# Kernel tuning notes

Hardware: AMD Instinct MI355X
Metric: run time of the kernel (lower is better)

Reference implementation:

```python
import jax, jax.numpy as jnp
import numpy as np

N = 1024
IN_F = 256
OUT_F = 128
H = 4
NH = OUT_F // H  # 32
NEG_SLOPE = 0.2


def setup_inputs() -> dict:
    key = jax.random.key(0)
    k1, k2, k3, k4, k5 = jax.random.split(key, 5)
    h = jax.random.normal(k1, (N, IN_F), dtype=jnp.float32)
    adj_mat = jax.random.randint(k2, (N, N, 1), 0, 2, dtype=jnp.int32)
    s_in = 1.0 / np.sqrt(IN_F)
    s_nh = 1.0 / np.sqrt(NH)
    Wl = jax.random.uniform(k3, (H * NH, IN_F), jnp.float32, -s_in, s_in)
    Wr = jax.random.uniform(k4, (H * NH, IN_F), jnp.float32, -s_in, s_in)
    attn_w = jax.random.uniform(k5, (NH,), jnp.float32, -s_nh, s_nh)
    return {"h": h, "adj_mat": adj_mat, "Wl": Wl, "Wr": Wr, "attn_w": attn_w}


def reference(h, adj_mat, Wl, Wr, attn_w):
    n = h.shape[0]
    g_l = (h @ Wl.T).reshape(n, H, NH)  # [N,H,F]
    g_r = (h @ Wr.T).reshape(n, H, NH)  # [N,H,F]
    # g_sum[i, j] = g_l[j] + g_r[i]  (repeat / repeat_interleave semantics)
    g_sum = g_l[None, :, :, :] + g_r[:, None, :, :]  # [N,N,H,F]
    act = jnp.where(g_sum >= 0, g_sum, NEG_SLOPE * g_sum)
    e = jnp.einsum('ijhf,f->ijh', act, attn_w)  # [N,N,H]
    mask = adj_mat != 0  # [N,N,1] broadcasts over heads
    e = jnp.where(mask, e, -jnp.inf)
    a = jax.nn.softmax(e, axis=1)  # softmax over source nodes j
    h_prime = jnp.einsum('ijh,jhf->ihf', a, g_r).reshape(n, H * NH)
    # is_output_layer=False -> ELU (dropout is a no-op in eval)
    return jax.nn.elu(h_prime)
```

## Files before the change

### kernel.cpp

```cpp
#include <hip/hip_runtime.h>
#include <math.h>

typedef float v2f __attribute__((ext_vector_type(2)));

#define NN 1024
#define IN_F 256
#define OUT_F 128
#define NHEADS 4
#define NHF 32

__global__ void __launch_bounds__(256) glr_gemm(const float* __restrict__ hmat,
                                                const float* __restrict__ Wl,
                                                const float* __restrict__ Wr,
                                                v2f* __restrict__ glT,
                                                float* __restrict__ grh) {
    __shared__ float hs[64 * 132];
    const int tid  = threadIdx.x;
    const int rg   = blockIdx.x;
    const int cs   = blockIdx.y;
    const int lane = tid & 63;
    const int wu   = __builtin_amdgcn_readfirstlane(tid >> 6);
    const int c0   = cs * 8 + wu * 2;
    const int half = c0 >> 7;
    const int cc   = c0 & 127;
    const float* __restrict__ W   = half ? Wr : Wl;
    const float* __restrict__ wr0 = W + cc * IN_F;
    const float* __restrict__ wr1 = wr0 + IN_F;

    float a0 = 0.f, a1 = 0.f;
    for (int kh = 0; kh < 2; ++kh) {
#pragma unroll
        for (int s = 0; s < 8; ++s) {
            const int v = tid + s * 256;
            const int row = v >> 5, q = v & 31;
            const float4 x = ((const float4*)hmat)[(rg * 64 + row) * 64 + kh * 32 + q];
            *(float4*)(hs + row * 132 + q * 4) = x;
        }
        __syncthreads();
        const float4* __restrict__ w0p = (const float4*)(wr0 + kh * 128);
        const float4* __restrict__ w1p = (const float4*)(wr1 + kh * 128);
        const float*  __restrict__ hrow = hs + lane * 132;
#pragma unroll 8
        for (int q = 0; q < 32; ++q) {
            const float4 hv = *(const float4*)(hrow + q * 4);
            const float4 w0 = w0p[q];
            const float4 w1 = w1p[q];
            a0 = fmaf(hv.x, w0.x, fmaf(hv.y, w0.y, fmaf(hv.z, w0.z, fmaf(hv.w, w0.w, a0))));
            a1 = fmaf(hv.x, w1.x, fmaf(hv.y, w1.y, fmaf(hv.z, w1.z, fmaf(hv.w, w1.w, a1))));
        }
        __syncthreads();
    }

    const int row = rg * 64 + lane;
    const int hh = cc >> 5, f0 = cc & 31;
    if (half == 0) {
        glT[(hh * 16 + (f0 >> 1)) * NN + row] = (v2f){a0, a1};
    } else {
        *(v2f*)(grh + (hh * NN + row) * NHF + f0) = (v2f){a0, a1};
    }
}

__global__ void __launch_bounds__(512, 4) gat_main(const v2f* __restrict__ glT,
                                                   const float* __restrict__ grh,
                                                   const int* __restrict__ adj,
                                                   const float* __restrict__ attn_w,
                                                   float* __restrict__ out) {
    const int hh  = blockIdx.y;
    const int i0  = blockIdx.x * 8;
    const int tid = threadIdx.x;

    __shared__ float p_buf[NN * 12];
    __shared__ float g_t[128 * 36];
    __shared__ float red[8][8];
    __shared__ float l_sh[8];

    const v2f* __restrict__ w2p = (const v2f*)attn_w;

    float lpart[8];
#pragma unroll
    for (int ii = 0; ii < 8; ++ii) lpart[ii] = 0.f;

    for (int c = 0; c < 2; ++c) {
        const int j = (c << 9) + tid;
        const v2f* __restrict__ glp = glT + hh * 16 * NN + j;
        v2f gl2[16];
#pragma unroll
        for (int fp = 0; fp < 16; ++fp) gl2[fp] = glp[fp * NN];

        v2f aa = {0.f, 0.f};
#pragma unroll
        for (int fp = 0; fp < 16; ++fp) aa += gl2[fp] * w2p[fp];
        const float alpha6 = 0.6f * (aa.x + aa.y);

        int adjv[8];
#pragma unroll
        for (int ii = 0; ii < 8; ++ii) adjv[ii] = adj[(i0 + ii) * NN + j];

        float pv[8];
#pragma unroll
        for (int ii = 0; ii < 8; ++ii) {
            const v2f* __restrict__ gr2 = (const v2f*)(grh + (hh * NN + i0 + ii) * NHF);
            v2f S = {0.f, 0.f};
#pragma unroll
            for (int fp = 0; fp < 16; ++fp) {
                const v2f s = gl2[fp] + gr2[fp];
                const v2f m = __builtin_elementwise_max(s, -s);
                S += m * w2p[fp];
            }
            const float e = fmaf(0.4f, S.x + S.y, alpha6);
            const float p = adjv[ii] ? __expf(e) : 0.f;
            pv[ii] = p;
            lpart[ii] += p;
        }
        float4 wA; wA.x = pv[0]; wA.y = pv[1]; wA.z = pv[2]; wA.w = pv[3];
        float4 wB; wB.x = pv[4]; wB.y = pv[5]; wB.z = pv[6]; wB.w = pv[7];
        *(float4*)&p_buf[j * 12]     = wA;
        *(float4*)&p_buf[j * 12 + 4] = wB;
    }

    const int lane = tid & 63, wv = tid >> 6;
#pragma unroll
    for (int ii = 0; ii < 8; ++ii) {
        float v = lpart[ii];
#pragma unroll
        for (int d = 32; d > 0; d >>= 1) v += __shfl_xor(v, d);
        if (lane == 0) red[ii][wv] = v;
    }
    __syncthreads();
    if (tid < 8) {
        float l = red[tid][0];
#pragma unroll
        for (int w = 1; w < 8; ++w) l += red[tid][w];
        l_sh[tid] = l;
    }
    __syncthreads();

    v2f acc[8][2];
#pragma unroll
    for (int ii = 0; ii < 8; ++ii) { acc[ii][0] = (v2f){0.f, 0.f}; acc[ii][1] = (v2f){0.f, 0.f}; }

    for (int t = 0; t < 8; ++t) {
        const float4* __restrict__ src = (const float4*)(grh + (hh * NN + t * 128) * NHF);
#pragma unroll
        for (int s2 = 0; s2 < 2; ++s2) {
            const int u = tid + s2 * 512;
            const int jj = u >> 3, f4 = u & 7;
            const float4 x = src[u];
            *(float4*)&g_t[jj * 36 + f4 * 4] = x;
        }
        __syncthreads();
#pragma unroll
        for (int u2 = 0; u2 < 2; ++u2) {
            const int jl = lane + (u2 << 6);
            const float* __restrict__ pb = &p_buf[(t * 128 + jl) * 12];
            const float4 pA = *(const float4*)pb;
            const float4 pB = *(const float4*)(pb + 4);
            const float4 g  = *(const float4*)&g_t[jl * 36 + wv * 4];
            const v2f g01 = {g.x, g.y}, g23 = {g.z, g.w};
            acc[0][0] += (v2f){pA.x, pA.x} * g01;  acc[0][1] += (v2f){pA.x, pA.x} * g23;
            acc[1][0] += (v2f){pA.y, pA.y} * g01;  acc[1][1] += (v2f){pA.y, pA.y} * g23;
            acc[2][0] += (v2f){pA.z, pA.z} * g01;  acc[2][1] += (v2f){pA.z, pA.z} * g23;
            acc[3][0] += (v2f){pA.w, pA.w} * g01;  acc[3][1] += (v2f){pA.w, pA.w} * g23;
            acc[4][0] += (v2f){pB.x, pB.x} * g01;  acc[4][1] += (v2f){pB.x, pB.x} * g23;
            acc[5][0] += (v2f){pB.y, pB.y} * g01;  acc[5][1] += (v2f){pB.y, pB.y} * g23;
            acc[6][0] += (v2f){pB.z, pB.z} * g01;  acc[6][1] += (v2f){pB.z, pB.z} * g23;
            acc[7][0] += (v2f){pB.w, pB.w} * g01;  acc[7][1] += (v2f){pB.w, pB.w} * g23;
        }
        __syncthreads();
    }

    float o32[32];
#pragma unroll
    for (int ii = 0; ii < 8; ++ii) {
        o32[ii * 4 + 0] = acc[ii][0].x;  o32[ii * 4 + 1] = acc[ii][0].y;
        o32[ii * 4 + 2] = acc[ii][1].x;  o32[ii * 4 + 3] = acc[ii][1].y;
    }
#pragma unroll
    for (int d = 32; d > 0; d >>= 1) {
#pragma unroll
        for (int k = 0; k < 32; ++k) o32[k] += __shfl_xor(o32[k], d);
    }
    if (lane == 0) {
#pragma unroll
        for (int ii = 0; ii < 8; ++ii) {
            const float inv = 1.f / l_sh[ii];
            float x0 = o32[ii * 4 + 0] * inv;
            float x1 = o32[ii * 4 + 1] * inv;
            float x2 = o32[ii * 4 + 2] * inv;
            float x3 = o32[ii * 4 + 3] * inv;
            float4 r;
            r.x = (x0 > 0.f) ? x0 : (__expf(x0) - 1.f);
            r.y = (x1 > 0.f) ? x1 : (__expf(x1) - 1.f);
            r.z = (x2 > 0.f) ? x2 : (__expf(x2) - 1.f);
            r.w = (x3 > 0.f) ? x3 : (__expf(x3) - 1.f);
            *(float4*)(out + (i0 + ii) * OUT_F + hh * NHF + wv * 4) = r;
        }
    }
}

extern "C" void kernel_launch(void* const* d_in, const int* in_sizes, int n_in,
                              void* d_out, int out_size, void* d_ws, size_t ws_size,
                              hipStream_t stream) {
    const float* hmat = (const float*)d_in[0];
    const int*   adj  = (const int*)d_in[1];
    const float* Wl   = (const float*)d_in[2];
    const float* Wr   = (const float*)d_in[3];
    const float* aw   = (const float*)d_in[4];
    float* o          = (float*)d_out;

    float* wsf = (float*)d_ws;
    v2f*   glT = (v2f*)wsf;
    float* grh = wsf + NHEADS * 16 * NN * 2;

    glr_gemm<<<dim3(16, 32), dim3(256), 0, stream>>>(hmat, Wl, Wr, glT, grh);
    gat_main<<<dim3(NN / 8, NHEADS), dim3(512), 0, stream>>>(glT, grh, adj, aw, o);
}
```

Baseline: 107.5 us.

## Remap attention scoring to one wave per target row with shared alpha

The score phase now gives each wavefront a single target row i and has it sweep all source nodes in 64-wide chunks. The g_r row is kept in registers, and the per-source alpha term is precomputed once into shared memory. The softmax denominator becomes a wave-local shuffle reduction, which removes the block-wide reduction and its extra barriers. p_buf is relaid as [8][NN] and the g_t padding stride changes to 33. The trade-off is that every wave now reloads the full g_l for the head, about eight times more global/L2 traffic, and float4 LDS reads at a stride of 33 are not 16-byte aligned.

```diff
diff --git a/kernel.cpp b/kernel.cpp
--- a/kernel.cpp
+++ b/kernel.cpp
@@ -65,108 +65,93 @@
                                                    const int* __restrict__ adj,
                                                    const float* __restrict__ attn_w,
                                                    float* __restrict__ out) {
-    const int hh  = blockIdx.y;
-    const int i0  = blockIdx.x * 8;
-    const int tid = threadIdx.x;
-
-    __shared__ float p_buf[NN * 12];
-    __shared__ float g_t[128 * 36];
-    __shared__ float red[8][8];
+    const int hh   = blockIdx.y;
+    const int i0   = blockIdx.x * 8;
+    const int tid  = threadIdx.x;
+    const int lane = tid & 63;
+    const int wv   = __builtin_amdgcn_readfirstlane(tid >> 6);
+
+    __shared__ float p_buf[8][NN];
+    __shared__ float alpha_s[NN];
+    __shared__ float g_t[128 * 33];
     __shared__ float l_sh[8];
 
-    const v2f* __restrict__ w2p = (const v2f*)attn_w;
-
-    float lpart[8];
-#pragma unroll
-    for (int ii = 0; ii < 8; ++ii) lpart[ii] = 0.f;
-
+    const v2f* __restrict__ w2p    = (const v2f*)attn_w;
+    const v2f* __restrict__ glbase = glT + hh * 16 * NN;
+
+#pragma unroll
     for (int c = 0; c < 2; ++c) {
         const int j = (c << 9) + tid;
-        const v2f* __restrict__ glp = glT + hh * 16 * NN + j;
+        const v2f* __restrict__ glp = glbase + j;
+        v2f aa = {0.f, 0.f};
+#pragma unroll
+        for (int fp = 0; fp < 16; ++fp) aa += glp[fp * NN] * w2p[fp];
+        alpha_s[j] = 0.6f * (aa.x + aa.y);
+    }
+
+    const v2f* __restrict__ gr2 = (const v2f*)(grh + (hh * NN + i0 + wv) * NHF);
+    v2f grr[16];
+#pragma unroll
+    for (int fp = 0; fp < 16; ++fp) grr[fp] = gr2[fp];
+
+    __syncthreads();
+
+    const int* __restrict__ adjrow = adj + (i0 + wv) * NN;
+    float lsum = 0.f;
+    for (int t = 0; t < 16; ++t) {
+        const int j = (t << 6) + lane;
+        const v2f* __restrict__ glp = glbase + j;
         v2f gl2[16];
 #pragma unroll
         for (int fp = 0; fp < 16; ++fp) gl2[fp] = glp[fp * NN];
-
-        v2f aa = {0.f, 0.f};
-#pragma unroll
-        for (int fp = 0; fp < 16; ++fp) aa += gl2[fp] * w2p[fp];
-        const float alpha6 = 0.6f * (aa.x + aa.y);
-
-        int adjv[8];
-#pragma unroll
-        for (int ii = 0; ii < 8; ++ii) adjv[ii] = adj[(i0 + ii) * NN + j];
-
-        float pv[8];
-#pragma unroll
-        for (int ii = 0; ii < 8; ++ii) {
-            const v2f* __restrict__ gr2 = (const v2f*)(grh + (hh * NN + i0 + ii) * NHF);
-            v2f S = {0.f, 0.f};
-#pragma unroll
-            for (int fp = 0; fp < 16; ++fp) {
-                const v2f s = gl2[fp] + gr2[fp];
-                const v2f m = __builtin_elementwise_max(s, -s);
-                S += m * w2p[fp];
-            }
-            const float e = fmaf(0.4f, S.x + S.y, alpha6);
-            const float p = adjv[ii] ? __expf(e) : 0.f;
-            pv[ii] = p;
-            lpart[ii] += p;
-        }
-        float4 wA; wA.x = pv[0]; wA.y = pv[1]; wA.z = pv[2]; wA.w = pv[3];
-        float4 wB; wB.x = pv[4]; wB.y = pv[5]; wB.z = pv[6]; wB.w = pv[7];
-        *(float4*)&p_buf[j * 12]     = wA;
-        *(float4*)&p_buf[j * 12 + 4] = wB;
-    }
-
-    const int lane = tid & 63, wv = tid >> 6;
-#pragma unroll
-    for (int ii = 0; ii < 8; ++ii) {
-        float v = lpart[ii];
-#pragma unroll
-        for (int d = 32; d > 0; d >>= 1) v += __shfl_xor(v, d);
-        if (lane == 0) red[ii][wv] = v;
-    }
-    __syncthreads();
-    if (tid < 8) {
-        float l = red[tid][0];
-#pragma unroll
-        for (int w = 1; w < 8; ++w) l += red[tid][w];
-        l_sh[tid] = l;
-    }
-    __syncthreads();
+        const int ad = adjrow[j];
+        v2f S = {0.f, 0.f};
+#pragma unroll
+        for (int fp = 0; fp < 16; ++fp) {
+            const v2f s = gl2[fp] + grr[fp];
+            const v2f m = __builtin_elementwise_max(s, -s);
+            S += m * w2p[fp];
+        }
+        const float e = fmaf(0.4f, S.x + S.y, alpha_s[j]);
+        const float p = ad ? __expf(e) : 0.f;
+        p_buf[wv][j] = p;
+        lsum += p;
+    }
+#pragma unroll
+    for (int d = 32; d > 0; d >>= 1) lsum += __shfl_xor(lsum, d);
+    if (lane == 0) l_sh[wv] = lsum;
 
     v2f acc[8][2];
 #pragma unroll
     for (int ii = 0; ii < 8; ++ii) { acc[ii][0] = (v2f){0.f, 0.f}; acc[ii][1] = (v2f){0.f, 0.f}; }
 
+    const float4* __restrict__ gsrc = (const float4*)(grh + hh * NN * NHF);
     for (int t = 0; t < 8; ++t) {
-        const float4* __restrict__ src = (const float4*)(grh + (hh * NN + t * 128) * NHF);
+        __syncthreads();
 #pragma unroll
         for (int s2 = 0; s2 < 2; ++s2) {
-            const int u = tid + s2 * 512;
+            const int u = tid + (s2 << 9);
             const int jj = u >> 3, f4 = u & 7;
-            const float4 x = src[u];
-            *(float4*)&g_t[jj * 36 + f4 * 4] = x;
+            const float4 x = gsrc[(t << 10) + u];
+            *(float4*)&g_t[jj * 33 + (f4 << 2)] = x;
         }
         __syncthreads();
 #pragma unroll
         for (int u2 = 0; u2 < 2; ++u2) {
             const int jl = lane + (u2 << 6);
-            const float* __restrict__ pb = &p_buf[(t * 128 + jl) * 12];
-            const float4 pA = *(const float4*)pb;
-            const float4 pB = *(const float4*)(pb + 4);
-            const float4 g  = *(const float4*)&g_t[jl * 36 + wv * 4];
+            const float4 g = *(const float4*)&g_t[jl * 33 + (wv << 2)];
+            const int jg = (t << 7) + jl;
+            float pv[8];
+#pragma unroll
+            for (int ii = 0; ii < 8; ++ii) pv[ii] = p_buf[ii][jg];
             const v2f g01 = {g.x, g.y}, g23 = {g.z, g.w};
-            acc[0][0] += (v2f){pA.x, pA.x} * g01;  acc[0][1] += (v2f){pA.x, pA.x} * g23;
-            acc[1][0] += (v2f){pA.y, pA.y} * g01;  acc[1][1] += (v2f){pA.y, pA.y} * g23;
-            acc[2][0] += (v2f){pA.z, pA.z} * g01;  acc[2][1] += (v2f){pA.z, pA.z} * g23;
-            acc[3][0] += (v2f){pA.w, pA.w} * g01;  acc[3][1] += (v2f){pA.w, pA.w} * g23;
-            acc[4][0] += (v2f){pB.x, pB.x} * g01;  acc[4][1] += (v2f){pB.x, pB.x} * g23;
-            acc[5][0] += (v2f){pB.y, pB.y} * g01;  acc[5][1] += (v2f){pB.y, pB.y} * g23;
-            acc[6][0] += (v2f){pB.z, pB.z} * g01;  acc[6][1] += (v2f){pB.z, pB.z} * g23;
-            acc[7][0] += (v2f){pB.w, pB.w} * g01;  acc[7][1] += (v2f){pB.w, pB.w} * g23;
-        }
-        __syncthreads();
+#pragma unroll
+            for (int ii = 0; ii < 8; ++ii) {
+                const v2f pp = {pv[ii], pv[ii]};
+                acc[ii][0] += pp * g01;
+                acc[ii][1] += pp * g23;
+            }
+        }
     }
 
     float o32[32];
@@ -184,16 +169,16 @@
 #pragma unroll
         for (int ii = 0; ii < 8; ++ii) {
             const float inv = 1.f / l_sh[ii];
-            float x0 = o32[ii * 4 + 0] * inv;
-            float x1 = o32[ii * 4 + 1] * inv;
-            float x2 = o32[ii * 4 + 2] * inv;
-            float x3 = o32[ii * 4 + 3] * inv;
+            const float x0 = o32[ii * 4 + 0] * inv;
+            const float x1 = o32[ii * 4 + 1] * inv;
+            const float x2 = o32[ii * 4 + 2] * inv;
+            const float x3 = o32[ii * 4 + 3] * inv;
             float4 r;
             r.x = (x0 > 0.f) ? x0 : (__expf(x0) - 1.f);
             r.y = (x1 > 0.f) ? x1 : (__expf(x1) - 1.f);
             r.z = (x2 > 0.f) ? x2 : (__expf(x2) - 1.f);
             r.w = (x3 > 0.f) ? x3 : (__expf(x3) - 1.f);
-            *(float4*)(out + (i0 + ii) * OUT_F + hh * NHF + wv * 4) = r;
+            *(float4*)(out + (i0 + ii) * OUT_F + hh * NHF + (wv << 2)) = r;
         }
     }
 }
```

After: 118.3 us. +10.1%, slower.
